# Optimization experiments

Hardware: AMD Instinct MI355X
Metric: run time of the kernel (lower is better)

Reference implementation:

```python
import jax, jax.numpy as jnp
import numpy as np

BS, N, INP, HID, REP, NPROTO, DEG, TOPK = 16, 4096, 64, 128, 128, 64, 8, 5
TAU_PROTO, SINK_EPS, SINK_ITERS = 0.3, 0.05, 20


def _l2(a, axis):
    n = jnp.linalg.norm(a, axis=axis, keepdims=True)
    return a / jnp.maximum(n, 1e-12)


def setup_inputs() -> dict:
    key = jax.random.key(0)
    ks = jax.random.split(key, 20)
    w = lambda k, shape, fan_in: jax.random.normal(k, shape, jnp.float32) / np.sqrt(fan_in)
    x = jax.random.normal(ks[0], (BS, N, INP), jnp.float32)
    y = jax.random.normal(ks[1], (BS, N, INP), jnp.float32)
    # structured ring edges: every node has DEG out/in neighbors (>= TOPK after diag fill)
    src = np.repeat(np.arange(N), DEG)
    dst = (src + np.tile(np.arange(1, DEG + 1), N)) % N
    edge_index = jnp.asarray(np.stack([src, dst]), dtype=jnp.int32)
    edge_weight = jax.random.uniform(ks[2], (N * DEG,), jnp.float32, 0.1, 1.0)
    krig_idx = jax.random.randint(ks[3], (BS, 256), 0, N, jnp.int32)
    perm_bs = jax.random.permutation(ks[4], BS).astype(jnp.int32)
    perm_nodes = jax.random.permutation(ks[5], N).astype(jnp.int32)
    Wproto = _l2(w(ks[6], (NPROTO, REP), REP), 1)  # torch copies row-normalized weight back into the param
    return {
        'x': x, 'y': y, 'edge_weight': edge_weight,
        'Wp1': w(ks[7], (INP, INP), INP), 'bp1': jnp.zeros((INP,), jnp.float32),
        'Wl1': w(ks[8], (HID, INP), INP), 'bl1': jnp.zeros((HID,), jnp.float32),
        'Wr1': w(ks[9], (HID, INP), INP),
        'Wp2': w(ks[10], (HID, HID), HID), 'bp2': jnp.zeros((HID,), jnp.float32),
        'Wl2': w(ks[11], (REP, HID), HID), 'bl2': jnp.zeros((REP,), jnp.float32),
        'Wr2': w(ks[12], (REP, HID), HID),
        'Wenc': w(ks[13], (REP, REP), REP), 'benc': jnp.zeros((REP,), jnp.float32),
        'Wproto': Wproto,
        'Wsa': w(ks[14], (1, REP), REP), 'bsa': jnp.zeros((1,), jnp.float32),
        'Wnc': w(ks[15], (REP, REP), REP), 'bnc': jnp.zeros((REP,), jnp.float32),
        'edge_index': edge_index, 'krig_idx': krig_idx,
        'perm_bs': perm_bs, 'perm_nodes': perm_nodes,
    }


def _sage(h, Wp, bp, Wl, bl, Wr, src, dst):
    # PyG SAGEConv(project=True, aggr='mean'): project+relu, mean-aggregate messages, root skip (no bias on lin_r)
    hp = jax.nn.relu(h @ Wp.T + bp)                      # [bs, N, din]
    agg = jnp.zeros_like(hp).at[:, dst].add(hp[:, src])  # scatter-add over edges
    cnt = jnp.zeros((h.shape[1],), h.dtype).at[dst].add(1.0)
    agg = agg / jnp.maximum(cnt, 1.0)[None, :, None]
    return agg @ Wl.T + bl + h @ Wr.T


def _encode(h, src, dst, Wp1, bp1, Wl1, bl1, Wr1, Wp2, bp2, Wl2, bl2, Wr2, Wenc, benc):
    h = jax.nn.relu(_sage(h, Wp1, bp1, Wl1, bl1, Wr1, src, dst))
    h = jax.nn.relu(_sage(h, Wp2, bp2, Wl2, bl2, Wr2, src, dst))
    return h @ Wenc.T + benc  # [bs, N, REP]


def _sinkhorn(out):
    Q = jnp.exp(out / SINK_EPS).T  # [K, B]
    Q = Q / Q.sum()
    K, B = Q.shape
    for _ in range(SINK_ITERS):  # fixed small iteration count
        Q = Q / Q.sum(axis=1, keepdims=True) / K
        Q = Q / Q.sum(axis=0, keepdims=True) / B
    return (Q * B).T


def _forward(x, y, edge_weight, Wp1, bp1, Wl1, bl1, Wr1, Wp2, bp2, Wl2, bl2, Wr2,
             Wenc, benc, Wproto, Wsa, bsa, Wnc, bnc,
             edge_index, krig_idx, perm_bs, perm_nodes):
    del krig_idx  # local_feat gather exists in torch but is dead w.r.t. the returned loss
    src, dst = edge_index[0], edge_index[1]
    enc = lambda h: _encode(h, src, dst, Wp1, bp1, Wl1, bl1, Wr1,
                            Wp2, bp2, Wl2, bl2, Wr2, Wenc, benc)
    z1 = enc(y)  # input.y view
    z2 = enc(x)  # input.x view

    # PrototypeHead (SwAV-style); prototype rows pre-normalized in setup, sinkhorn targets are detached
    zc1 = _l2(z1.reshape(-1, REP), 1) @ Wproto.T
    zc2 = _l2(z2.reshape(-1, REP), 1) @ Wproto.T
    q1 = jax.lax.stop_gradient(_sinkhorn(zc1))
    q2 = jax.lax.stop_gradient(_sinkhorn(zc2))
    l1 = -jnp.mean(jnp.sum(q1 * jax.nn.log_softmax(zc2 / TAU_PROTO, axis=1), axis=1))
    l2 = -jnp.mean(jnp.sum(q2 * jax.nn.log_softmax(zc1 / TAU_PROTO, axis=1), axis=1))
    loss1 = l1 + l2

    # NeigborContrast.neighbor_readout, vectorized: dense adj -> per-row top-5 -> attention aggregate
    adj = jnp.zeros((N, N), x.dtype).at[src, dst].set(edge_weight)
    diag = jnp.arange(N)
    adj = adj.at[diag, diag].set(1.0)  # fill_diagonal_(1)
    masked = jnp.where(adj > 0, adj, -jnp.inf)
    _, topk_idx = jax.lax.top_k(masked, TOPK)  # [N, TOPK] neighbor ids by weight (desc)
    nbs = z1[:, topk_idx]  # [bs, N, TOPK, REP] gather
    att = jax.nn.softmax(jnp.squeeze(nbs @ Wsa.T + bsa, -1), axis=-1)  # [bs, N, TOPK]
    ans = jnp.einsum('bnkd,bnk->bnd', nbs, att) @ Wnc.T + bnc
    shuf = ans[perm_bs][:, perm_nodes]

    # Discriminator: cosine score per node (= diagonal of bmm(s, h^T) after L2-normalize)
    s, hr, hf = _l2(z2, -1), _l2(ans, -1), _l2(shuf, -1)
    sc_rl = jnp.sum(s * hr, axis=-1)  # [bs, N]
    sc_fk = jnp.sum(s * hf, axis=-1)
    logits = jnp.concatenate([sc_rl, sc_fk], axis=1)  # [bs, 2N]
    lbl = jnp.concatenate([jnp.ones_like(sc_rl), jnp.zeros_like(sc_fk)], axis=1)
    loss2 = jnp.mean(lbl * jax.nn.softplus(-logits) + (1.0 - lbl) * jax.nn.softplus(logits))
    acc = jnp.mean(((jax.nn.sigmoid(logits) > 0.5) == (lbl > 0.5)).astype(jnp.float32))
    return loss1 + loss2, acc


def reference(x, y, edge_weight, Wp1, bp1, Wl1, bl1, Wr1, Wp2, bp2, Wl2, bl2, Wr2,
              Wenc, benc, Wproto, Wsa, bsa, Wnc, bnc,
              edge_index, krig_idx, perm_bs, perm_nodes):
    return _forward(x, y, edge_weight, Wp1, bp1, Wl1, bl1, Wr1, Wp2, bp2, Wl2, bl2, Wr2,
                    Wenc, benc, Wproto, Wsa, bsa, Wnc, bnc,
                    edge_index, krig_idx, perm_bs, perm_nodes)
```

## Files before the change

kernel.cpp:

```cpp
#include <hip/hip_runtime.h>
#include <math.h>

#define NN 4096
#define EE 65536
#define E2 (2*EE)
#define DEG 8
#define NPROTO 64
#define REP 128
#define TOPKK 5
#define SINKI 20
#define SB 256

typedef __attribute__((ext_vector_type(8))) short short8;
typedef __attribute__((ext_vector_type(4))) float f32x4;
typedef __attribute__((ext_vector_type(8))) __bf16 bf16x8;
typedef __attribute__((ext_vector_type(4))) unsigned short us4;
typedef unsigned short u16;
typedef unsigned int u32;

__device__ __forceinline__ float b2f(u32 u){
  union { float f; u32 i; } v; v.i = u<<16; return v.f;
}
__device__ __forceinline__ u16 f2b(float f){
  __bf16 h = (__bf16)f;
// ... 5 lines not shown
__device__ __forceinline__ us4 pk4(float a, float b, float c, float d){
  us4 o; o.x=f2b(a); o.y=f2b(b); o.z=f2b(c); o.w=f2b(d); return o;
}
__device__ __forceinline__ f32x4 MFMA_BF16(short8 a, short8 b, f32x4 c){
  return __builtin_amdgcn_mfma_f32_16x16x32_bf16(
      __builtin_bit_cast(bf16x8, a), __builtin_bit_cast(bf16x8, b), c, 0, 0, 0);
}
__device__ __forceinline__ void stage16(const u16* g, u16* l){
  typedef __attribute__((address_space(1))) const unsigned int gu32;
  typedef __attribute__((address_space(3))) unsigned int lu32;
  __builtin_amdgcn_global_load_lds((gu32*)g, (lu32*)l, 16, 0, 0);
}
__device__ __forceinline__ float wsum(float v){
  #pragma unroll
  for(int m=32;m>=1;m>>=1) v += __shfl_xor(v,m);
  return v;
}
__device__ __forceinline__ float r16sum(float v){
  #pragma unroll
  for(int m=8;m>=1;m>>=1) v += __shfl_xor(v,m);
  return v;
}
__device__ __forceinline__ float softplusf(float x){
  if(x > 20.f) return x;
  if(x < -20.f) return __expf(x);
  return log1pf(__expf(x));
}

__global__ __launch_bounds__(256) void k_prep(
    const int* __restrict__ ei, const float* __restrict__ ew, int* __restrict__ topk,
    const float* __restrict__ Wp1, const float* __restrict__ Wl1, const float* __restrict__ Wr1,
    const float* __restrict__ Wp2, const float* __restrict__ Wl2, const float* __restrict__ Wr2,
    const float* __restrict__ Wenc, const float* __restrict__ Wproto, const float* __restrict__ Wnc,
    u16* __restrict__ Wp1b, u16* __restrict__ Wc1b, u16* __restrict__ Wp2b, u16* __restrict__ Wc2b,
    u16* __restrict__ Wencb, u16* __restrict__ Wprotob, u16* __restrict__ Wncb,
    const float* __restrict__ x, const float* __restrict__ y, u16* __restrict__ XY){
  const int NW = 4096+16384+16384+32768+16384+8192+16384;
  const int N4 = EE*64/4;
  const int TOTAL = 4096 + NW + 2*N4;
  for(int t0 = blockIdx.x*256+threadIdx.x; t0 < TOTAL; t0 += gridDim.x*256){
    int t = t0;
    if(t < 4096){
      int i = t;
      float val[DEG+1]; int idx[DEG+1]; bool used[DEG+1];
      val[0] = 1.0f; idx[0] = i; used[0]=false;
      for(int k=0;k<DEG;k++){
        int e = i*DEG + k;
        val[k+1] = ew[e];
        idx[k+1] = ei[NN*DEG + e];
        used[k+1] = false;
      }
      for(int s=0;s<TOPKK;s++){
        int best = -1;
        for(int k=0;k<=DEG;k++){
          if(used[k]) continue;
          if(best<0 || val[k]>val[best] || (val[k]==val[best] && idx[k]<idx[best])) best=k;
        }
        used[best]=true;
        topk[i*TOPKK+s]=idx[best];
      }
      continue;
    }
    t -= 4096;
    if(t < NW){
      if(t < 4096){ Wp1b[t]=f2b(Wp1[t]); continue; } t-=4096;
      if(t < 16384){ int c=t>>7, k=t&127;
        Wc1b[t]=f2b(k<64? Wl1[c*64+k] : Wr1[c*64+k-64]); continue; } t-=16384;
      if(t < 16384){ Wp2b[t]=f2b(Wp2[t]); continue; } t-=16384;
      if(t < 32768){ int c=t>>8, k=t&255;
        Wc2b[t]=f2b(k<128? Wl2[c*128+k] : Wr2[c*128+k-128]); continue; } t-=32768;
      if(t < 16384){ Wencb[t]=f2b(Wenc[t]); continue; } t-=16384;
      if(t < 8192){ Wprotob[t]=f2b(Wproto[t]); continue; } t-=8192;
      Wncb[t]=f2b(Wnc[t]); continue;
    }
    t -= NW;
    const float* s = (t<N4)? y : x;
    int k = (t<N4)? t : t-N4;
    float4 v = ((const float4*)s)[k];
    ((us4*)XY)[t] = pk4(v.x, v.y, v.z, v.w);
  }
}

__global__ __launch_bounds__(256)
void k_f123(const u16* __restrict__ XY,
            const u16* __restrict__ Wp1b, const float* __restrict__ bp1,
            const u16* __restrict__ Wc1b, const float* __restrict__ bl1,
            const u16* __restrict__ Wp2b, const float* __restrict__ bp2,
            u16* __restrict__ H1, u16* __restrict__ HP2){
  __shared__ __align__(16) char arena[53248];
  u16* A  = (u16*)arena;
  u16* B  = (u16*)(arena + 18432);
  u16* C  = (u16*)(arena + 36864);
  u16* T  = (u16*)(arena + 18432);
  const int tid = threadIdx.x;
  const int w = tid>>6, l = tid&63;
  const int lr = l&15, kg = l>>4;
  const int rw = w&1, cw = w>>1;
  const int rowoff = rw*64, cbase = cw*64;
  const long rb0 = (long)blockIdx.x*128;
  const long n0 = rb0 & (NN-1), sbase = rb0 - n0;

  for(int c=w;c<18;c+=4){
    int off=c*1024+l*16, row=off>>7;
    int cu=(off&127)^((row&7)<<4);
    long gn=(n0-8+row)&(NN-1);
    stage16(XY+(sbase+gn)*64+(cu>>1), A+c*512);
  }
  __syncthreads();

  for(int t=w; t<9; t+=4){
    f32x4 acc1[4];
    #pragma unroll
    for(int cf=0;cf<4;cf++) acc1[cf]=(f32x4){0.f,0.f,0.f,0.f};
    const char* base = (const char*)A + (t*16+lr)*128;
    const int sw=(lr&7)<<4;
    short8 af0 = *(const short8*)(base + ((kg*16)^sw));
    short8 af1 = *(const short8*)(base + ((64+kg*16)^sw));
    #pragma unroll
    for(int cf=0;cf<4;cf++){
      int ch=cf*16+lr;
      short8 wf0 = *(const short8*)(Wp1b + ch*64 + kg*8);
      short8 wf1 = *(const short8*)(Wp1b + ch*64 + 32 + kg*8);
      acc1[cf]=MFMA_BF16(wf0, af0, acc1[cf]);
      acc1[cf]=MFMA_BF16(wf1, af1, acc1[cf]);
    }
    int row=t*16+lr;
    #pragma unroll
    for(int cf=0;cf<4;cf++){
      int c0=cf*16+kg*4;
      float4 bv=*(const float4*)(bp1+c0);
      us4 o = pk4(fmaxf(acc1[cf][0]+bv.x,0.f), fmaxf(acc1[cf][1]+bv.y,0.f),
                  fmaxf(acc1[cf][2]+bv.z,0.f), fmaxf(acc1[cf][3]+bv.w,0.f));
      *(us4*)((char*)B + row*128 + ((c0*2)^((row&7)<<4))) = o;
    }
  }
  __syncthreads();

  {
    const int s=tid>>5, cp=tid&31;
    float a0=0.f,a1=0.f;
    #pragma unroll
    for(int t2=0;t2<8;t2++){
      int r=s*16+t2;
      u32 v=((const u32*)B)[r*32+(cp^((r&7)<<2))];
      a0+=b2f(v&0xffffu); a1+=b2f(v>>16);
    }
    #pragma unroll
    for(int i=0;i<16;i++){
      int r=s*16+i;
      ((u32*)C)[r*32+(cp^((r&7)<<2))] = pk2(a0*0.125f, a1*0.125f);
      u32 va=((const u32*)B)[(r+8)*32+(cp^((r&7)<<2))];
      u32 vs=((const u32*)B)[r*32+(cp^((r&7)<<2))];
      a0+=b2f(va&0xffffu)-b2f(vs&0xffffu);
      a1+=b2f(va>>16)-b2f(vs>>16);
    }
  }
  __syncthreads();

  f32x4 acc[4][4];
  #pragma unroll
  for(int a=0;a<4;a++)
    #pragma unroll
    for(int b=0;b<4;b++) acc[a][b]=(f32x4){0.f,0.f,0.f,0.f};
  #pragma unroll
  for(int kc=0;kc<2;kc++){
    const char* Ab = kc? ((const char*)A + 8*128) : (const char*)C;
    short8 af[4][2];
    #pragma unroll
    for(int f=0;f<4;f++){
      const char* base = Ab + (rowoff+f*16+lr)*128;
      const int sw = (lr&7)<<4;
      af[f][0] = *(const short8*)(base + ((kg*16)^sw));
      af[f][1] = *(const short8*)(base + ((64+kg*16)^sw));
    }
    #pragma unroll
    for(int cf=0;cf<4;cf++){
      const int ch = cbase + cf*16 + lr;
      short8 wf0 = *(const short8*)(Wc1b + (long)ch*128 + kc*64 + kg*8);
      short8 wf1 = *(const short8*)(Wc1b + (long)ch*128 + kc*64 + 32 + kg*8);
      #pragma unroll
      for(int f=0;f<4;f++){
        acc[cf][f] = MFMA_BF16(wf0, af[f][0], acc[cf][f]);
        acc[cf][f] = MFMA_BF16(wf1, af[f][1], acc[cf][f]);
      }
    }
  }
  __syncthreads();

  #pragma unroll
  for(int f=0;f<4;f++){
    const int row = rowoff + f*16 + lr;
    #pragma unroll
    for(int cf=0;cf<4;cf++){
      const int c0 = cbase + cf*16 + kg*4;
      float4 bv = *(const float4*)(bl1 + c0);
      us4 o = pk4(fmaxf(acc[cf][f][0]+bv.x,0.f), fmaxf(acc[cf][f][1]+bv.y,0.f),
                  fmaxf(acc[cf][f][2]+bv.z,0.f), fmaxf(acc[cf][f][3]+bv.w,0.f));
      *(us4*)(H1 + (rb0+row)*128 + c0) = o;
      *(us4*)((char*)T + row*256 + ((c0*2)^((row&7)<<4))) = o;
    }
  }
  __syncthreads();

  #pragma unroll
  for(int a=0;a<4;a++)
    #pragma unroll
    for(int b=0;b<4;b++) acc[a][b]=(f32x4){0.f,0.f,0.f,0.f};
  #pragma unroll
  for(int kc=0;kc<2;kc++){
    short8 af[4][2];
    #pragma unroll
    for(int f=0;f<4;f++){
      const char* base = (const char*)T + (rowoff+f*16+lr)*256;
      const int sw = (lr&7)<<4;
      af[f][0] = *(const short8*)(base + ((kc*128+kg*16)^sw));
      af[f][1] = *(const short8*)(base + ((kc*128+64+kg*16)^sw));
    }
    #pragma unroll
    for(int cf=0;cf<4;cf++){
      const int ch = cbase + cf*16 + lr;
      short8 wf0 = *(const short8*)(Wp2b + (long)ch*128 + kc*64 + kg*8);
      short8 wf1 = *(const short8*)(Wp2b + (long)ch*128 + kc*64 + 32 + kg*8);
      #pragma unroll
      for(int f=0;f<4;f++){
        acc[cf][f] = MFMA_BF16(wf0, af[f][0], acc[cf][f]);
        acc[cf][f] = MFMA_BF16(wf1, af[f][1], acc[cf][f]);
      }
    }
  }
  #pragma unroll
  for(int f=0;f<4;f++){
    const long row = rb0 + rowoff + f*16 + lr;
    #pragma unroll
    for(int cf=0;cf<4;cf++){
      const int c0 = cbase + cf*16 + kg*4;
      float4 bv = *(const float4*)(bp2 + c0);
      us4 o = pk4(fmaxf(acc[cf][f][0]+bv.x,0.f), fmaxf(acc[cf][f][1]+bv.y,0.f),
                  fmaxf(acc[cf][f][2]+bv.z,0.f), fmaxf(acc[cf][f][3]+bv.w,0.f));
      *(us4*)(HP2 + row*128 + c0) = o;
    }
  }
}

__global__ __launch_bounds__(256)
void k_f456(const u16* __restrict__ HP2, const u16* __restrict__ H1,
            const u16* __restrict__ Wc2b, const float* __restrict__ bl2,
            const u16* __restrict__ Wencb, const float* __restrict__ benc,
            const u16* __restrict__ Wprotob,
            u16* __restrict__ Z, float* __restrict__ INVN, u16* __restrict__ Mout){
  __shared__ __align__(16) char arena[67584];
  u16* h0 = (u16*)arena;
  u16* h1 = (u16*)(arena + 17408);
  u16* a2 = (u16*)(arena + 34816);
  u16* a3 = (u16*)(arena + 51200);
  u16* T  = (u16*)arena;
  __shared__ float lnorm[2][128];
  const int tid = threadIdx.x;
  const int w = tid>>6, l = tid&63;
  const int lr = l&15, kg = l>>4;
  const int rw = w&1, cw = w>>1;
  const int rowoff = rw*64, cbase = cw*64;
  const long rb0 = (long)blockIdx.x*128;
  const long n0 = rb0 & (NN-1), sbase = rb0 - n0;

  for(int c=w;c<17;c+=4){
    int off=c*1024+l*16, row=off>>7, colb=off&127;
    long gn=(n0-8+row)&(NN-1);
    stage16(HP2+(sbase+gn)*128+(colb>>1), h0+c*512);
    stage16(HP2+(sbase+gn)*128+32+(colb>>1), h1+c*512);
  }
  for(int c=w;c<16;c+=4){
    int off=c*1024+l*16, row=off>>7;
    int cu=(off&127)^((row&7)<<4);
    stage16(H1+(rb0+row)*128+(cu>>1), a2+c*512);
    stage16(H1+(rb0+row)*128+64+(cu>>1), a3+c*512);
  }
  __syncthreads();

  u32 o0v[16], o1v[16];
  {
    const int s = tid>>5, cp = tid&31;
    const u32* r0 = (const u32*)h0;
    const u32* r1 = (const u32*)h1;
    float a00=0.f,a01=0.f,a10=0.f,a11=0.f;
    #pragma unroll
    for(int t=0;t<8;t++){
      u32 v0=r0[(s*16+t)*32+cp]; a00+=b2f(v0&0xffffu); a01+=b2f(v0>>16);
      u32 v1=r1[(s*16+t)*32+cp]; a10+=b2f(v1&0xffffu); a11+=b2f(v1>>16);
    }
    #pragma unroll
    for(int i=0;i<16;i++){
      int r=s*16+i;
      o0v[i]=pk2(a00*0.125f, a01*0.125f);
      o1v[i]=pk2(a10*0.125f, a11*0.125f);
      u32 va0=r0[(r+8)*32+cp], vs0=r0[r*32+cp];
      a00+=b2f(va0&0xffffu)-b2f(vs0&0xffffu);
      a01+=b2f(va0>>16)-b2f(vs0>>16);
      u32 va1=r1[(r+8)*32+cp], vs1=r1[r*32+cp];
      a10+=b2f(va1&0xffffu)-b2f(vs1&0xffffu);
      a11+=b2f(va1>>16)-b2f(vs1>>16);
    }
    __syncthreads();
    u32* w0=(u32*)h0; u32* w1=(u32*)h1;
    #pragma unroll
    for(int i=0;i<16;i++){
      int r=s*16+i;
      int idx=r*32+(cp^((r&7)<<2));
      w0[idx]=o0v[i];
      w1[idx]=o1v[i];
    }
  }
  __syncthreads();

  f32x4 acc[4][4];
  #pragma unroll
  for(int a=0;a<4;a++)
    #pragma unroll
    for(int b=0;b<4;b++) acc[a][b]=(f32x4){0.f,0.f,0.f,0.f};
  #pragma unroll
  for(int kc=0;kc<4;kc++){
    const char* Ab = (kc==0)? (const char*)h0 : (kc==1)? (const char*)h1
                   : (kc==2)? (const char*)a2 : (const char*)a3;
    short8 af[4][2];
    #pragma unroll
    for(int f=0;f<4;f++){
      const char* base = Ab + (rowoff+f*16+lr)*128;
      const int sw = (lr&7)<<4;
      af[f][0] = *(const short8*)(base + ((kg*16)^sw));
      af[f][1] = *(const short8*)(base + ((64+kg*16)^sw));
    }
    #pragma unroll
    for(int cf=0;cf<4;cf++){
      const int ch = cbase + cf*16 + lr;
      short8 wf0 = *(const short8*)(Wc2b + (long)ch*256 + kc*64 + kg*8);
      short8 wf1 = *(const short8*)(Wc2b + (long)ch*256 + kc*64 + 32 + kg*8);
      #pragma unroll
      for(int f=0;f<4;f++){
        acc[cf][f] = MFMA_BF16(wf0, af[f][0], acc[cf][f]);
        acc[cf][f] = MFMA_BF16(wf1, af[f][1], acc[cf][f]);
      }
    }
  }
  __syncthreads();

  #pragma unroll
  for(int f=0;f<4;f++){
    const int row = rowoff + f*16 + lr;
    #pragma unroll
    for(int cf=0;cf<4;cf++){
      const int c0 = cbase + cf*16 + kg*4;
      float4 bv = *(const float4*)(bl2 + c0);
      us4 o = pk4(fmaxf(acc[cf][f][0]+bv.x,0.f), fmaxf(acc[cf][f][1]+bv.y,0.f),
                  fmaxf(acc[cf][f][2]+bv.z,0.f), fmaxf(acc[cf][f][3]+bv.w,0.f));
      *(us4*)((char*)T + row*256 + ((c0*2)^((row&7)<<4))) = o;
    }
  }
  __syncthreads();

  #pragma unroll
  for(int a=0;a<4;a++)
    #pragma unroll
    for(int b=0;b<4;b++) acc[a][b]=(f32x4){0.f,0.f,0.f,0.f};
  #pragma unroll
  for(int kc=0;kc<2;kc++){
    short8 af[4][2];
    #pragma unroll
    for(int f=0;f<4;f++){
      const char* base = (const char*)T + (rowoff+f*16+lr)*256;
      const int sw = (lr&7)<<4;
      af[f][0] = *(const short8*)(base + ((kc*128+kg*16)^sw));
      af[f][1] = *(const short8*)(base + ((kc*128+64+kg*16)^sw));
    }
    #pragma unroll
    for(int cf=0;cf<4;cf++){
      const int ch = cbase + cf*16 + lr;
      short8 wf0 = *(const short8*)(Wencb + (long)ch*128 + kc*64 + kg*8);
      short8 wf1 = *(const short8*)(Wencb + (long)ch*128 + kc*64 + 32 + kg*8);
      #pragma unroll
      for(int f=0;f<4;f++){
        acc[cf][f] = MFMA_BF16(wf0, af[f][0], acc[cf][f]);
        acc[cf][f] = MFMA_BF16(wf1, af[f][1], acc[cf][f]);
      }
    }
  }
  __syncthreads();

  {
    float sn[4] = {0.f,0.f,0.f,0.f};
    #pragma unroll
    for(int f=0;f<4;f++){
      #pragma unroll
      for(int cf=0;cf<4;cf++){
        const int c0 = cbase + cf*16 + kg*4;
        float4 bv = *(const float4*)(benc + c0);
        float v0=acc[cf][f][0]+bv.x, v1=acc[cf][f][1]+bv.y;
        float v2=acc[cf][f][2]+bv.z, v3=acc[cf][f][3]+bv.w;
        sn[f] += v0*v0+v1*v1+v2*v2+v3*v3;
      }
      float s = sn[f];
      s += __shfl_xor(s, 16);
      s += __shfl_xor(s, 32);
      if(kg==0) lnorm[cw][rw*64 + f*16 + lr] = s;
    }
  }
  __syncthreads();
  if(tid < 128){
    float s = lnorm[0][tid] + lnorm[1][tid];
    INVN[rb0 + tid] = 1.0f/fmaxf(sqrtf(s), 1e-12f);
  }
  #pragma unroll
  for(int f=0;f<4;f++){
    const int row = rowoff + f*16 + lr;
    float sr = lnorm[0][row] + lnorm[1][row];
    float inv = 1.0f/fmaxf(sqrtf(sr), 1e-12f);
    #pragma unroll
    for(int cf=0;cf<4;cf++){
      const int c0 = cbase + cf*16 + kg*4;
      float4 bv = *(const float4*)(benc + c0);
      float v0=acc[cf][f][0]+bv.x, v1=acc[cf][f][1]+bv.y;
      float v2=acc[cf][f][2]+bv.z, v3=acc[cf][f][3]+bv.w;
      *(us4*)(Z + (rb0+row)*128 + c0) = pk4(v0,v1,v2,v3);
      *(us4*)((char*)T + row*256 + ((c0*2)^((row&7)<<4))) = pk4(v0*inv,v1*inv,v2*inv,v3*inv);
    }
  }
  __syncthreads();

  f32x4 acc3[2][4];
  #pragma unroll
  for(int a=0;a<2;a++)
    #pragma unroll
    for(int b=0;b<4;b++) acc3[a][b]=(f32x4){0.f,0.f,0.f,0.f};
  #pragma unroll
  for(int kc=0;kc<2;kc++){
    short8 af[4][2];
    #pragma unroll
    for(int f=0;f<4;f++){
      const char* base = (const char*)T + (rowoff+f*16+lr)*256;
      const int sw = (lr&7)<<4;
      af[f][0] = *(const short8*)(base + ((kc*128+kg*16)^sw));
      af[f][1] = *(const short8*)(base + ((kc*128+64+kg*16)^sw));
    }
    #pragma unroll
    for(int cf=0;cf<2;cf++){
      const int ch = cw*32 + cf*16 + lr;
      short8 wf0 = *(const short8*)(Wprotob + (long)ch*128 + kc*64 + kg*8);
      short8 wf1 = *(const short8*)(Wprotob + (long)ch*128 + kc*64 + 32 + kg*8);
      #pragma unroll
      for(int f=0;f<4;f++){
        acc3[cf][f] = MFMA_BF16(wf0, af[f][0], acc3[cf][f]);
        acc3[cf][f] = MFMA_BF16(wf1, af[f][1], acc3[cf][f]);
      }
    }
  }
  #pragma unroll
  for(int f=0;f<4;f++){
    const long row = rb0 + rowoff + f*16 + lr;
    #pragma unroll
    for(int cf=0;cf<2;cf++){
      const int c0 = cw*32 + cf*16 + kg*4;
      *(us4*)(Mout + row*64 + c0) = pk4(__expf(20.f*acc3[cf][f][0]), __expf(20.f*acc3[cf][f][1]),
                                        __expf(20.f*acc3[cf][f][2]), __expf(20.f*acc3[cf][f][3]));
    }
  }
}

__global__ __launch_bounds__(256)
void k_sink2(const u16* __restrict__ M, const float* __restrict__ Pdprev,
             float* __restrict__ Pdcur, int it){
  __shared__ float T[4][64*33];
  __shared__ float ulds[NPROTO];
  __shared__ float redw[4][NPROTO];
  const int tid = threadIdx.x, b = blockIdx.x;
  const int wv = tid>>6, l = tid&63;
  const int mat = b>>8, bi = b&255;
  const long row = (long)mat*EE + (long)bi*256 + wv*64 + l;

  float m[64];
  #pragma unroll
  for(int j=0;j<8;j++){
    short8 v = *(const short8*)(M + row*64 + j*8);
    #pragma unroll
    for(int e=0;e<8;e++) m[j*8+e] = b2f((u16)v[e]);
  }

  if(it > 0 && tid < 128){
    int k = tid>>1, half = tid&1;
    const float4* src = (const float4*)(Pdprev + (long)(mat*64+k)*SB + half*128);
    float s = 0.f;
    #pragma unroll
    for(int j=0;j<32;j++){ float4 q = src[j]; s += q.x+q.y+q.z+q.w; }
    s += __shfl_xor(s, 1);
    if(half==0) ulds[k] = 1.0f/((float)NPROTO * s);
  }
  __syncthreads();

  float vv = 1.f;
  if(it > 0){
    float s = 0.f;
    #pragma unroll
    for(int k=0;k<64;k++) s += m[k]*ulds[k];
    vv = 1.0f/((float)EE * s);
  }

  float* Tw = &T[wv][0];
  const int col = l&31, rh = l>>5;
  #pragma unroll
  for(int h=0;h<2;h++){
    #pragma unroll
    for(int kk=0;kk<32;kk++) Tw[l*33+kk] = m[h*32+kk]*vv;
    __syncthreads();
    float s = 0.f;
    #pragma unroll
    for(int j=0;j<32;j++) s += Tw[(rh*32+j)*33 + col];
    s += __shfl_xor(s, 32);
    if(l<32) redw[wv][h*32+l] = s;
    __syncthreads();
  }
  if(tid < 64){
    float s = redw[0][tid]+redw[1][tid]+redw[2][tid]+redw[3][tid];
    Pdcur[(long)(mat*64+tid)*SB + bi] = s;
  }
}

// ... 180 lines not shown
                                               float2* __restrict__ p2){
  const int tid = threadIdx.x, wv = tid>>6;
  const int gw = blockIdx.x*4 + wv;
  const int l = tid&63, g = l>>4, li = l&15;
  const int nw = gridDim.x*4;
  float lsum=0.f, asum=0.f;
  for(long r0 = (long)gw*4; r0 < EE; r0 += (long)nw*4){
    long r = r0 + g;
    int b = (int)(r>>12), n = (int)(r&(NN-1));
    long rfrow = (long)pb[b]*NN + pn[n];
    uint4 zv = ((const uint4*)(Z2 + r*REP))[li];
    uint4 av = ((const uint4*)(ANS + r*REP))[li];
    uint4 fv = ((const uint4*)(ANS + rfrow*REP))[li];
    float sr=0.f, sf=0.f;
    {
      u32 za[4]={zv.x,zv.y,zv.z,zv.w}, aa[4]={av.x,av.y,av.z,av.w}, fa[4]={fv.x,fv.y,fv.z,fv.w};
      #pragma unroll
      for(int j=0;j<4;j++){
        float z0=b2f(za[j]&0xffffu), z1=b2f(za[j]>>16);
        sr += z0*b2f(aa[j]&0xffffu) + z1*b2f(aa[j]>>16);
        sf += z0*b2f(fa[j]&0xffffu) + z1*b2f(fa[j]>>16);
      }
    }
    sr = r16sum(sr); sf = r16sum(sf);
    if(li==0){
      float in2 = invn2[r];
      float scrl = sr*in2*ansn[r];
      float scfk = sf*in2*ansn[rfrow];
      lsum += softplusf(-scrl) + softplusf(scfk);
      asum += (scrl>0.f?1.f:0.f) + (scfk>0.f?0.f:1.f);
    }
  }
  lsum = wsum(lsum); asum = wsum(asum);
  __shared__ float rl[4], ra[4];
  if(l==0){ rl[wv]=lsum; ra[wv]=asum; }
  __syncthreads();
  if(tid==0){
    float2 o; o.x=rl[0]+rl[1]+rl[2]+rl[3]; o.y=ra[0]+ra[1]+ra[2]+ra[3];
    p2[blockIdx.x]=o;
  }
}

__global__ void k_final(const float* __restrict__ p1, const float2* __restrict__ p2,
                        int n1, int n2, float* __restrict__ out){
  int l = threadIdx.x;
  double s1=0,s2=0,sa=0;
  for(int i=l;i<n1;i+=64) s1 += (double)p1[i];
  for(int i=l;i<n2;i+=64){ float2 v=p2[i]; s2+=(double)v.x; sa+=(double)v.y; }
  #pragma unroll
  for(int m=32;m>=1;m>>=1){ s1+=__shfl_xor(s1,m); s2+=__shfl_xor(s2,m); sa+=__shfl_xor(sa,m); }
  if(l==0){
    double loss1 = -s1/(double)EE;
    double loss2 = s2/(double)(2*EE);
    double acc   = sa/(double)(2*EE);
    out[0]=(float)(loss1+loss2);
    out[1]=(float)acc;
  }
}

extern "C" void kernel_launch(void* const* d_in, const int* in_sizes, int n_in,
                              void* d_out, int out_size, void* d_ws, size_t ws_size,
                              hipStream_t stream){
  const float* x   = (const float*)d_in[0];
  const float* y   = (const float*)d_in[1];
  const float* ew  = (const float*)d_in[2];
  const float* Wp1=(const float*)d_in[3];  const float* bp1=(const float*)d_in[4];
  const float* Wl1=(const float*)d_in[5];  const float* bl1=(const float*)d_in[6];
  const float* Wr1=(const float*)d_in[7];
  const float* Wp2=(const float*)d_in[8];  const float* bp2=(const float*)d_in[9];
  const float* Wl2=(const float*)d_in[10]; const float* bl2=(const float*)d_in[11];
  const float* Wr2=(const float*)d_in[12];
  const float* Wenc=(const float*)d_in[13]; const float* benc=(const float*)d_in[14];
  const float* Wproto=(const float*)d_in[15];
  const float* Wsa=(const float*)d_in[16]; const float* bsa=(const float*)d_in[17];
  const float* Wnc=(const float*)d_in[18]; const float* bnc=(const float*)d_in[19];
  const int* ei=(const int*)d_in[20];
  const int* pb=(const int*)d_in[22];
  const int* pn=(const int*)d_in[23];

  char* p = (char*)d_ws;
  auto carve=[&](size_t b)->void*{ void* r=(void*)p; p += (b+255)&~(size_t)255; return r; };
  u16* XY  = (u16*)carve((size_t)E2*64*2);
  u16* S2  = (u16*)carve((size_t)E2*REP*2);
  u16* S1b = (u16*)carve((size_t)E2*REP*2);
  u16* Z   = (u16*)carve((size_t)E2*REP*2);
  u16* M   = (u16*)carve((size_t)E2*NPROTO*2);
  float* INVN=(float*)carve((size_t)E2*4);
  float* ANSN=(float*)carve((size_t)EE*4);
  u16* Wp1b = (u16*)carve(64*64*2);
  u16* Wc1b = (u16*)carve(128*128*2);
  u16* Wp2b = (u16*)carve(128*128*2);
  u16* Wc2b = (u16*)carve((size_t)128*256*2);
  u16* Wencb= (u16*)carve(128*128*2);
  u16* Wprotob=(u16*)carve(64*128*2);
  u16* Wncb = (u16*)carve(128*128*2);
  int* topk = (int*)carve((size_t)NN*TOPKK*4);
  float* Pd = (float*)carve((size_t)SINKI*128*SB*4);
  float* D  = (float*)carve(128*4);
  float* P1 = (float*)carve(1024*4);
  float2* P2 = (float2*)carve(1024*8);
  if((size_t)(p - (char*)d_ws) > ws_size) return;

  u16* Z1 = Z;
  u16* Z2 = Z + (size_t)EE*REP;
  u16* M1 = M;
  u16* M2 = M + (size_t)EE*NPROTO;
  float* INVN2 = INVN + EE;

  k_prep<<<2048,256,0,stream>>>(ei, ew, topk,
      Wp1,Wl1,Wr1,Wp2,Wl2,Wr2,Wenc,Wproto,Wnc,
      Wp1b,Wc1b,Wp2b,Wc2b,Wencb,Wprotob,Wncb,
      x, y, XY);

  k_f123<<<E2/128,256,0,stream>>>(XY, Wp1b, bp1, Wc1b, bl1, Wp2b, bp2, S2, S1b);
  k_f456<<<E2/128,256,0,stream>>>(S1b, S2, Wc2b, bl2, Wencb, benc, Wprotob, Z, INVN, M);

  for(int it=0; it<SINKI; ++it)
    k_sink2<<<512,256,0,stream>>>(M, Pd + (long)(it-1)*128*SB, Pd + (long)it*128*SB, it);
  k_ufinal<<<1,256,0,stream>>>(Pd + (long)(SINKI-1)*128*SB, D);
  k_loss1<<<1024,256,0,stream>>>(M1, M2, D, D+64, P1);

  k_attnc<<<EE/128,256,0,stream>>>(Z1, topk, Wsa, bsa, Wncb, bnc, S2, ANSN);
  k_loss2<<<1024,256,0,stream>>>(Z2, S2, INVN2, ANSN, pb, pn, P2);

  k_final<<<1,64,0,stream>>>(P1, P2, 1024, 1024, (float*)d_out);
}
```

Measured before the change: 356.3 us.

## Fuse both encoder kernels into one with halo recomputation in LDS

Merges k_f123 and k_f456 into one kernel, k_enc. It stages a 16-row neighbour halo and recomputes the first SAGE layer and the projection for those halo rows, so the second ring-mean aggregation can run entirely in shared memory. This removes the global write and re-read of the H1 and HP2 intermediates, and one kernel launch. In exchange it does extra matmul work on the halo rows and uses a larger LDS arena of about 78KB, which may lower occupancy.

Result: slower. 375.5 us (+5.4%).

```diff
diff --git a/kernel.cpp b/kernel.cpp
--- a/kernel.cpp
+++ b/kernel.cpp
@@ -111,236 +111,202 @@
 }
 
 __global__ __launch_bounds__(256)
-void k_f123(const u16* __restrict__ XY,
-            const u16* __restrict__ Wp1b, const float* __restrict__ bp1,
-            const u16* __restrict__ Wc1b, const float* __restrict__ bl1,
-            const u16* __restrict__ Wp2b, const float* __restrict__ bp2,
-            u16* __restrict__ H1, u16* __restrict__ HP2){
-  __shared__ __align__(16) char arena[53248];
-  u16* A  = (u16*)arena;
-  u16* B  = (u16*)(arena + 18432);
-  u16* C  = (u16*)(arena + 36864);
-  u16* T  = (u16*)(arena + 18432);
+void k_enc(const u16* __restrict__ XY,
+           const u16* __restrict__ Wp1b, const float* __restrict__ bp1,
+           const u16* __restrict__ Wc1b, const float* __restrict__ bl1,
+           const u16* __restrict__ Wp2b, const float* __restrict__ bp2,
+           const u16* __restrict__ Wc2b, const float* __restrict__ bl2,
+           const u16* __restrict__ Wencb, const float* __restrict__ benc,
+           const u16* __restrict__ Wprotob,
+           u16* __restrict__ Z, float* __restrict__ INVN, u16* __restrict__ Mout){
+  __shared__ __align__(16) char arena[77824];
+  __shared__ float lnorm[2][128];
+  char* s0c = arena;
+  char* s1c = arena + 19456;
+  char* s2c = arena + 38912;
+  char* s3c = arena + 58368;
   const int tid = threadIdx.x;
   const int w = tid>>6, l = tid&63;
   const int lr = l&15, kg = l>>4;
-  const int rw = w&1, cw = w>>1;
-  const int rowoff = rw*64, cbase = cw*64;
   const long rb0 = (long)blockIdx.x*128;
   const long n0 = rb0 & (NN-1), sbase = rb0 - n0;
+  const int sw = (lr&7)<<4;
 
   for(int c=w;c<18;c+=4){
     int off=c*1024+l*16, row=off>>7;
     int cu=(off&127)^((row&7)<<4);
-    long gn=(n0-8+row)&(NN-1);
-    stage16(XY+(sbase+gn)*64+(cu>>1), A+c*512);
-  }
-  __syncthreads();
-
-  for(int t=w; t<9; t+=4){
-    f32x4 acc1[4];
-    #pragma unroll
-    for(int cf=0;cf<4;cf++) acc1[cf]=(f32x4){0.f,0.f,0.f,0.f};
-    const char* base = (const char*)A + (t*16+lr)*128;
-    const int sw=(lr&7)<<4;
+    long gn=(n0-16+row)&(NN-1);
+    stage16(XY+(sbase+gn)*64+(cu>>1), (u16*)s0c+c*512);
+  }
+  __syncthreads();
+
+  for(int g=w; g<9; g+=4){
+    const int row = g*16 + lr;
+    const char* base = s0c + row*128;
     short8 af0 = *(const short8*)(base + ((kg*16)^sw));
     short8 af1 = *(const short8*)(base + ((64+kg*16)^sw));
+    f32x4 a4[4];
     #pragma unroll
     for(int cf=0;cf<4;cf++){
+      a4[cf]=(f32x4){0.f,0.f,0.f,0.f};
       int ch=cf*16+lr;
       short8 wf0 = *(const short8*)(Wp1b + ch*64 + kg*8);
       short8 wf1 = *(const short8*)(Wp1b + ch*64 + 32 + kg*8);
-      acc1[cf]=MFMA_BF16(wf0, af0, acc1[cf]);
-      acc1[cf]=MFMA_BF16(wf1, af1, acc1[cf]);
-    }
-    int row=t*16+lr;
+      a4[cf]=MFMA_BF16(wf0, af0, a4[cf]);
+      a4[cf]=MFMA_BF16(wf1, af1, a4[cf]);
+    }
     #pragma unroll
     for(int cf=0;cf<4;cf++){
       int c0=cf*16+kg*4;
       float4 bv=*(const float4*)(bp1+c0);
-      us4 o = pk4(fmaxf(acc1[cf][0]+bv.x,0.f), fmaxf(acc1[cf][1]+bv.y,0.f),
-                  fmaxf(acc1[cf][2]+bv.z,0.f), fmaxf(acc1[cf][3]+bv.w,0.f));
-      *(us4*)((char*)B + row*128 + ((c0*2)^((row&7)<<4))) = o;
+      us4 o = pk4(fmaxf(a4[cf][0]+bv.x,0.f), fmaxf(a4[cf][1]+bv.y,0.f),
+                  fmaxf(a4[cf][2]+bv.z,0.f), fmaxf(a4[cf][3]+bv.w,0.f));
+      *(us4*)(s1c + row*128 + ((c0*2)^((row&7)<<4))) = o;
     }
   }
   __syncthreads();
 
   {
     const int s=tid>>5, cp=tid&31;
+    const u32* B = (const u32*)s1c;
+    u32* C = (u32*)s2c;
+    const int row0 = 8 + s*17;
     float a0=0.f,a1=0.f;
     #pragma unroll
-    for(int t2=0;t2<8;t2++){
-      int r=s*16+t2;
-      u32 v=((const u32*)B)[r*32+(cp^((r&7)<<2))];
+    for(int t=0;t<8;t++){
+      int r=row0-8+t;
+      u32 v=B[r*32+(cp^((r&7)<<2))];
       a0+=b2f(v&0xffffu); a1+=b2f(v>>16);
     }
     #pragma unroll
+    for(int i=0;i<17;i++){
+      int r=row0+i;
+      C[r*32+(cp^((r&7)<<2))] = pk2(a0*0.125f, a1*0.125f);
+      if(i<16){
+        u32 va=B[r*32+(cp^((r&7)<<2))];
+        u32 vs=B[(r-8)*32+(cp^((r&7)<<2))];
+        a0+=b2f(va&0xffffu)-b2f(vs&0xffffu);
+        a1+=b2f(va>>16)-b2f(vs>>16);
+      }
+    }
+  }
+  __syncthreads();
+
+  for(int g=w; g<9; g+=4){
+    const int row = 8 + g*16 + lr;
+    short8 afm[2], afx[2];
+    { const char* bm = s2c + row*128;
+      afm[0] = *(const short8*)(bm + ((kg*16)^sw));
+      afm[1] = *(const short8*)(bm + ((64+kg*16)^sw));
+      const char* bx = s0c + row*128;
+      afx[0] = *(const short8*)(bx + ((kg*16)^sw));
+      afx[1] = *(const short8*)(bx + ((64+kg*16)^sw)); }
+    f32x4 a8[8];
+    #pragma unroll
+    for(int cf=0;cf<8;cf++){
+      a8[cf]=(f32x4){0.f,0.f,0.f,0.f};
+      int ch=cf*16+lr;
+      short8 w0 = *(const short8*)(Wc1b + (long)ch*128 + kg*8);
+      short8 w1 = *(const short8*)(Wc1b + (long)ch*128 + 32 + kg*8);
+      short8 w2 = *(const short8*)(Wc1b + (long)ch*128 + 64 + kg*8);
+      short8 w3 = *(const short8*)(Wc1b + (long)ch*128 + 96 + kg*8);
+      a8[cf]=MFMA_BF16(w0, afm[0], a8[cf]);
+      a8[cf]=MFMA_BF16(w1, afm[1], a8[cf]);
+      a8[cf]=MFMA_BF16(w2, afx[0], a8[cf]);
+      a8[cf]=MFMA_BF16(w3, afx[1], a8[cf]);
+    }
+    if(row < 144){
+      #pragma unroll
+      for(int cf=0;cf<8;cf++){
+        int c0=cf*16+kg*4;
+        float4 bv=*(const float4*)(bl1+c0);
+        us4 o = pk4(fmaxf(a8[cf][0]+bv.x,0.f), fmaxf(a8[cf][1]+bv.y,0.f),
+                    fmaxf(a8[cf][2]+bv.z,0.f), fmaxf(a8[cf][3]+bv.w,0.f));
+        int cl = (cf&3)*16 + kg*4;
+        char* dst = (cf<4)? s1c : s3c;
+        *(us4*)(dst + row*128 + ((cl*2)^((row&7)<<4))) = o;
+      }
+    }
+  }
+  __syncthreads();
+
+  for(int g=w; g<9; g+=4){
+    const int row = 8 + g*16 + lr;
+    short8 afa[2], afb[2];
+    { const char* ba = s1c + row*128;
+      afa[0] = *(const short8*)(ba + ((kg*16)^sw));
+      afa[1] = *(const short8*)(ba + ((64+kg*16)^sw));
+      const char* bb = s3c + row*128;
+      afb[0] = *(const short8*)(bb + ((kg*16)^sw));
+      afb[1] = *(const short8*)(bb + ((64+kg*16)^sw)); }
+    f32x4 a8[8];
+    #pragma unroll
+    for(int cf=0;cf<8;cf++){
+      a8[cf]=(f32x4){0.f,0.f,0.f,0.f};
+      int ch=cf*16+lr;
+      short8 w0 = *(const short8*)(Wp2b + (long)ch*128 + kg*8);
+      short8 w1 = *(const short8*)(Wp2b + (long)ch*128 + 32 + kg*8);
+      short8 w2 = *(const short8*)(Wp2b + (long)ch*128 + 64 + kg*8);
+      short8 w3 = *(const short8*)(Wp2b + (long)ch*128 + 96 + kg*8);
+      a8[cf]=MFMA_BF16(w0, afa[0], a8[cf]);
+      a8[cf]=MFMA_BF16(w1, afa[1], a8[cf]);
+      a8[cf]=MFMA_BF16(w2, afb[0], a8[cf]);
+      a8[cf]=MFMA_BF16(w3, afb[1], a8[cf]);
+    }
+    if(row < 144){
+      #pragma unroll
+      for(int cf=0;cf<8;cf++){
+        int c0=cf*16+kg*4;
+        float4 bv=*(const float4*)(bp2+c0);
+        us4 o = pk4(fmaxf(a8[cf][0]+bv.x,0.f), fmaxf(a8[cf][1]+bv.y,0.f),
+                    fmaxf(a8[cf][2]+bv.z,0.f), fmaxf(a8[cf][3]+bv.w,0.f));
+        int cl = (cf&3)*16 + kg*4;
+        char* dst = (cf<4)? s0c : s2c;
+        *(us4*)(dst + row*128 + ((cl*2)^((row&7)<<4))) = o;
+      }
+    }
+  }
+  __syncthreads();
+
+  {
+    const int s=tid>>5, cp=tid&31;
+    const u32* B0 = (const u32*)s0c;
+    const u32* B1 = (const u32*)s2c;
+    const int row0 = 16 + s*16;
+    float a0=0.f,a1=0.f,c0=0.f,c1=0.f;
+    #pragma unroll
+    for(int t=0;t<8;t++){
+      int r=row0-8+t;
+      u32 v0=B0[r*32+(cp^((r&7)<<2))]; a0+=b2f(v0&0xffffu); a1+=b2f(v0>>16);
+      u32 v1=B1[r*32+(cp^((r&7)<<2))]; c0+=b2f(v1&0xffffu); c1+=b2f(v1>>16);
+    }
+    u32 oa[16], ob[16];
+    #pragma unroll
     for(int i=0;i<16;i++){
-      int r=s*16+i;
-      ((u32*)C)[r*32+(cp^((r&7)<<2))] = pk2(a0*0.125f, a1*0.125f);
-      u32 va=((const u32*)B)[(r+8)*32+(cp^((r&7)<<2))];
-      u32 vs=((const u32*)B)[r*32+(cp^((r&7)<<2))];
-      a0+=b2f(va&0xffffu)-b2f(vs&0xffffu);
-      a1+=b2f(va>>16)-b2f(vs>>16);
-    }
-  }
-  __syncthreads();
-
-  f32x4 acc[4][4];
-  #pragma unroll
-  for(int a=0;a<4;a++)
-    #pragma unroll
-    for(int b=0;b<4;b++) acc[a][b]=(f32x4){0.f,0.f,0.f,0.f};
-  #pragma unroll
-  for(int kc=0;kc<2;kc++){
-    const char* Ab = kc? ((const char*)A + 8*128) : (const char*)C;
-    short8 af[4][2];
-    #pragma unroll
-    for(int f=0;f<4;f++){
-      const char* base = Ab + (rowoff+f*16+lr)*128;
-      const int sw = (lr&7)<<4;
-      af[f][0] = *(const short8*)(base + ((kg*16)^sw));
-      af[f][1] = *(const short8*)(base + ((64+kg*16)^sw));
-    }
-    #pragma unroll
-    for(int cf=0;cf<4;cf++){
-      const int ch = cbase + cf*16 + lr;
-      short8 wf0 = *(const short8*)(Wc1b + (long)ch*128 + kc*64 + kg*8);
-      short8 wf1 = *(const short8*)(Wc1b + (long)ch*128 + kc*64 + 32 + kg*8);
-      #pragma unroll
-      for(int f=0;f<4;f++){
-        acc[cf][f] = MFMA_BF16(wf0, af[f][0], acc[cf][f]);
-        acc[cf][f] = MFMA_BF16(wf1, af[f][1], acc[cf][f]);
-      }
-    }
-  }
-  __syncthreads();
-
-  #pragma unroll
-  for(int f=0;f<4;f++){
-    const int row = rowoff + f*16 + lr;
-    #pragma unroll
-    for(int cf=0;cf<4;cf++){
-      const int c0 = cbase + cf*16 + kg*4;
-      float4 bv = *(const float4*)(bl1 + c0);
-      us4 o = pk4(fmaxf(acc[cf][f][0]+bv.x,0.f), fmaxf(acc[cf][f][1]+bv.y,0.f),
-                  fmaxf(acc[cf][f][2]+bv.z,0.f), fmaxf(acc[cf][f][3]+bv.w,0.f));
-      *(us4*)(H1 + (rb0+row)*128 + c0) = o;
-      *(us4*)((char*)T + row*256 + ((c0*2)^((row&7)<<4))) = o;
-    }
-  }
-  __syncthreads();
-
-  #pragma unroll
-  for(int a=0;a<4;a++)
-    #pragma unroll
-    for(int b=0;b<4;b++) acc[a][b]=(f32x4){0.f,0.f,0.f,0.f};
-  #pragma unroll
-  for(int kc=0;kc<2;kc++){
-    short8 af[4][2];
-    #pragma unroll
-    for(int f=0;f<4;f++){
-      const char* base = (const char*)T + (rowoff+f*16+lr)*256;
-      const int sw = (lr&7)<<4;
-      af[f][0] = *(const short8*)(base + ((kc*128+kg*16)^sw));
-      af[f][1] = *(const short8*)(base + ((kc*128+64+kg*16)^sw));
-    }
-    #pragma unroll
-    for(int cf=0;cf<4;cf++){
-      const int ch = cbase + cf*16 + lr;
-      short8 wf0 = *(const short8*)(Wp2b + (long)ch*128 + kc*64 + kg*8);
-      short8 wf1 = *(const short8*)(Wp2b + (long)ch*128 + kc*64 + 32 + kg*8);
-      #pragma unroll
-      for(int f=0;f<4;f++){
-        acc[cf][f] = MFMA_BF16(wf0, af[f][0], acc[cf][f]);
-        acc[cf][f] = MFMA_BF16(wf1, af[f][1], acc[cf][f]);
-      }
-    }
-  }
-  #pragma unroll
-  for(int f=0;f<4;f++){
-    const long row = rb0 + rowoff + f*16 + lr;
-    #pragma unroll
-    for(int cf=0;cf<4;cf++){
-      const int c0 = cbase + cf*16 + kg*4;
-      float4 bv = *(const float4*)(bp2 + c0);
-      us4 o = pk4(fmaxf(acc[cf][f][0]+bv.x,0.f), fmaxf(acc[cf][f][1]+bv.y,0.f),
-                  fmaxf(acc[cf][f][2]+bv.z,0.f), fmaxf(acc[cf][f][3]+bv.w,0.f));
-      *(us4*)(HP2 + row*128 + c0) = o;
-    }
-  }
-}
-
-__global__ __launch_bounds__(256)
-void k_f456(const u16* __restrict__ HP2, const u16* __restrict__ H1,
-            const u16* __restrict__ Wc2b, const float* __restrict__ bl2,
-            const u16* __restrict__ Wencb, const float* __restrict__ benc,
-            const u16* __restrict__ Wprotob,
-            u16* __restrict__ Z, float* __restrict__ INVN, u16* __restrict__ Mout){
-  __shared__ __align__(16) char arena[67584];
-  u16* h0 = (u16*)arena;
-  u16* h1 = (u16*)(arena + 17408);
-  u16* a2 = (u16*)(arena + 34816);
-  u16* a3 = (u16*)(arena + 51200);
-  u16* T  = (u16*)arena;
-  __shared__ float lnorm[2][128];
-  const int tid = threadIdx.x;
-  const int w = tid>>6, l = tid&63;
-  const int lr = l&15, kg = l>>4;
+      int r=row0+i;
+      oa[i]=pk2(a0*0.125f, a1*0.125f);
+      ob[i]=pk2(c0*0.125f, c1*0.125f);
+      u32 va0=B0[r*32+(cp^((r&7)<<2))], vs0=B0[(r-8)*32+(cp^((r&7)<<2))];
+      a0+=b2f(va0&0xffffu)-b2f(vs0&0xffffu);
+      a1+=b2f(va0>>16)-b2f(vs0>>16);
+      u32 va1=B1[r*32+(cp^((r&7)<<2))], vs1=B1[(r-8)*32+(cp^((r&7)<<2))];
+      c0+=b2f(va1&0xffffu)-b2f(vs1&0xffffu);
+      c1+=b2f(va1>>16)-b2f(vs1>>16);
+    }
+    __syncthreads();
+    u32* W0=(u32*)s0c; u32* W1=(u32*)s2c;
+    #pragma unroll
+    for(int i=0;i<16;i++){
+      int r=row0+i;
+      int idx=r*32+(cp^((r&7)<<2));
+      W0[idx]=oa[i];
+      W1[idx]=ob[i];
+    }
+  }
+  __syncthreads();
+
   const int rw = w&1, cw = w>>1;
   const int rowoff = rw*64, cbase = cw*64;
-  const long rb0 = (long)blockIdx.x*128;
-  const long n0 = rb0 & (NN-1), sbase = rb0 - n0;
-
-  for(int c=w;c<17;c+=4){
-    int off=c*1024+l*16, row=off>>7, colb=off&127;
-    long gn=(n0-8+row)&(NN-1);
-    stage16(HP2+(sbase+gn)*128+(colb>>1), h0+c*512);
-    stage16(HP2+(sbase+gn)*128+32+(colb>>1), h1+c*512);
-  }
-  for(int c=w;c<16;c+=4){
-    int off=c*1024+l*16, row=off>>7;
-    int cu=(off&127)^((row&7)<<4);
-    stage16(H1+(rb0+row)*128+(cu>>1), a2+c*512);
-    stage16(H1+(rb0+row)*128+64+(cu>>1), a3+c*512);
-  }
-  __syncthreads();
-
-  u32 o0v[16], o1v[16];
-  {
-    const int s = tid>>5, cp = tid&31;
-    const u32* r0 = (const u32*)h0;
-    const u32* r1 = (const u32*)h1;
-    float a00=0.f,a01=0.f,a10=0.f,a11=0.f;
-    #pragma unroll
-    for(int t=0;t<8;t++){
-      u32 v0=r0[(s*16+t)*32+cp]; a00+=b2f(v0&0xffffu); a01+=b2f(v0>>16);
-      u32 v1=r1[(s*16+t)*32+cp]; a10+=b2f(v1&0xffffu); a11+=b2f(v1>>16);
-    }
-    #pragma unroll
-    for(int i=0;i<16;i++){
-      int r=s*16+i;
-      o0v[i]=pk2(a00*0.125f, a01*0.125f);
-      o1v[i]=pk2(a10*0.125f, a11*0.125f);
-      u32 va0=r0[(r+8)*32+cp], vs0=r0[r*32+cp];
-      a00+=b2f(va0&0xffffu)-b2f(vs0&0xffffu);
-      a01+=b2f(va0>>16)-b2f(vs0>>16);
-      u32 va1=r1[(r+8)*32+cp], vs1=r1[r*32+cp];
-      a10+=b2f(va1&0xffffu)-b2f(vs1&0xffffu);
-      a11+=b2f(va1>>16)-b2f(vs1>>16);
-    }
-    __syncthreads();
-    u32* w0=(u32*)h0; u32* w1=(u32*)h1;
-    #pragma unroll
-    for(int i=0;i<16;i++){
-      int r=s*16+i;
-      int idx=r*32+(cp^((r&7)<<2));
-      w0[idx]=o0v[i];
-      w1[idx]=o1v[i];
-    }
-  }
-  __syncthreads();
-
   f32x4 acc[4][4];
   #pragma unroll
   for(int a=0;a<4;a++)
@@ -348,13 +314,11 @@
     for(int b=0;b<4;b++) acc[a][b]=(f32x4){0.f,0.f,0.f,0.f};
   #pragma unroll
   for(int kc=0;kc<4;kc++){
-    const char* Ab = (kc==0)? (const char*)h0 : (kc==1)? (const char*)h1
-                   : (kc==2)? (const char*)a2 : (const char*)a3;
+    const char* Ab = (kc==0)? s0c : (kc==1)? s2c : (kc==2)? s1c : s3c;
     short8 af[4][2];
     #pragma unroll
     for(int f=0;f<4;f++){
-      const char* base = Ab + (rowoff+f*16+lr)*128;
-      const int sw = (lr&7)<<4;
+      const char* base = Ab + (16+rowoff+f*16+lr)*128;
       af[f][0] = *(const short8*)(base + ((kg*16)^sw));
       af[f][1] = *(const short8*)(base + ((64+kg*16)^sw));
     }
@@ -374,14 +338,16 @@
 
   #pragma unroll
   for(int f=0;f<4;f++){
-    const int row = rowoff + f*16 + lr;
+    const int row = 16 + rowoff + f*16 + lr;
     #pragma unroll
     for(int cf=0;cf<4;cf++){
       const int c0 = cbase + cf*16 + kg*4;
       float4 bv = *(const float4*)(bl2 + c0);
       us4 o = pk4(fmaxf(acc[cf][f][0]+bv.x,0.f), fmaxf(acc[cf][f][1]+bv.y,0.f),
                   fmaxf(acc[cf][f][2]+bv.z,0.f), fmaxf(acc[cf][f][3]+bv.w,0.f));
-      *(us4*)((char*)T + row*256 + ((c0*2)^((row&7)<<4))) = o;
+      int cl = (c0 & 63)*2;
+      char* dst = (c0<64)? s0c : s1c;
+      *(us4*)(dst + row*128 + (cl^((row&7)<<4))) = o;
     }
   }
   __syncthreads();
@@ -392,13 +358,13 @@
     for(int b=0;b<4;b++) acc[a][b]=(f32x4){0.f,0.f,0.f,0.f};
   #pragma unroll
   for(int kc=0;kc<2;kc++){
+    const char* Ab = kc? s1c : s0c;
     short8 af[4][2];
     #pragma unroll
     for(int f=0;f<4;f++){
-      const char* base = (const char*)T + (rowoff+f*16+lr)*256;
-      const int sw = (lr&7)<<4;
-      af[f][0] = *(const short8*)(base + ((kc*128+kg*16)^sw));
-      af[f][1] = *(const short8*)(base + ((kc*128+64+kg*16)^sw));
+      const char* base = Ab + (16+rowoff+f*16+lr)*128;
+      af[f][0] = *(const short8*)(base + ((kg*16)^sw));
+      af[f][1] = *(const short8*)(base + ((64+kg*16)^sw));
     }
     #pragma unroll
     for(int cf=0;cf<4;cf++){
@@ -412,8 +378,6 @@
       }
     }
   }
-  __syncthreads();
-
   {
     float sn[4] = {0.f,0.f,0.f,0.f};
     #pragma unroll
@@ -429,7 +393,7 @@
       float s = sn[f];
       s += __shfl_xor(s, 16);
       s += __shfl_xor(s, 32);
-      if(kg==0) lnorm[cw][rw*64 + f*16 + lr] = s;
+      if(kg==0) lnorm[cw][rowoff + f*16 + lr] = s;
     }
   }
   __syncthreads();
@@ -439,8 +403,9 @@
   }
   #pragma unroll
   for(int f=0;f<4;f++){
-    const int row = rowoff + f*16 + lr;
-    float sr = lnorm[0][row] + lnorm[1][row];
+    const int orow = rowoff + f*16 + lr;
+    const int row = 16 + orow;
+    float sr = lnorm[0][orow] + lnorm[1][orow];
     float inv = 1.0f/fmaxf(sqrtf(sr), 1e-12f);
     #pragma unroll
     for(int cf=0;cf<4;cf++){
@@ -448,8 +413,10 @@
       float4 bv = *(const float4*)(benc + c0);
       float v0=acc[cf][f][0]+bv.x, v1=acc[cf][f][1]+bv.y;
       float v2=acc[cf][f][2]+bv.z, v3=acc[cf][f][3]+bv.w;
-      *(us4*)(Z + (rb0+row)*128 + c0) = pk4(v0,v1,v2,v3);
-      *(us4*)((char*)T + row*256 + ((c0*2)^((row&7)<<4))) = pk4(v0*inv,v1*inv,v2*inv,v3*inv);
+      *(us4*)(Z + (rb0+orow)*128 + c0) = pk4(v0,v1,v2,v3);
+      int cl = (c0 & 63)*2;
+      char* dst = (c0<64)? s2c : s3c;
+      *(us4*)(dst + row*128 + (cl^((row&7)<<4))) = pk4(v0*inv,v1*inv,v2*inv,v3*inv);
     }
   }
   __syncthreads();
@@ -461,13 +428,13 @@
     for(int b=0;b<4;b++) acc3[a][b]=(f32x4){0.f,0.f,0.f,0.f};
   #pragma unroll
   for(int kc=0;kc<2;kc++){
+    const char* Ab = kc? s3c : s2c;
     short8 af[4][2];
     #pragma unroll
     for(int f=0;f<4;f++){
-      const char* base = (const char*)T + (rowoff+f*16+lr)*256;
-      const int sw = (lr&7)<<4;
-      af[f][0] = *(const short8*)(base + ((kc*128+kg*16)^sw));
-      af[f][1] = *(const short8*)(base + ((kc*128+64+kg*16)^sw));
+      const char* base = Ab + (16+rowoff+f*16+lr)*128;
+      af[f][0] = *(const short8*)(base + ((kg*16)^sw));
+      af[f][1] = *(const short8*)(base + ((64+kg*16)^sw));
     }
     #pragma unroll
     for(int cf=0;cf<2;cf++){
@@ -814,7 +781,6 @@
   auto carve=[&](size_t b)->void*{ void* r=(void*)p; p += (b+255)&~(size_t)255; return r; };
   u16* XY  = (u16*)carve((size_t)E2*64*2);
   u16* S2  = (u16*)carve((size_t)E2*REP*2);
-  u16* S1b = (u16*)carve((size_t)E2*REP*2);
   u16* Z   = (u16*)carve((size_t)E2*REP*2);
   u16* M   = (u16*)carve((size_t)E2*NPROTO*2);
   float* INVN=(float*)carve((size_t)E2*4);
@@ -844,8 +810,8 @@
       Wp1b,Wc1b,Wp2b,Wc2b,Wencb,Wprotob,Wncb,
       x, y, XY);
 
-  k_f123<<<E2/128,256,0,stream>>>(XY, Wp1b, bp1, Wc1b, bl1, Wp2b, bp2, S2, S1b);
-  k_f456<<<E2/128,256,0,stream>>>(S1b, S2, Wc2b, bl2, Wencb, benc, Wprotob, Z, INVN, M);
+  k_enc<<<E2/128,256,0,stream>>>(XY, Wp1b, bp1, Wc1b, bl1, Wp2b, bp2,
+                                 Wc2b, bl2, Wencb, benc, Wprotob, Z, INVN, M);
 
   for(int it=0; it<SINKI; ++it)
     k_sink2<<<512,256,0,stream>>>(M, Pd + (long)(it-1)*128*SB, Pd + (long)it*128*SB, it);
```
